# Performance work log

Hardware: AMD Instinct MI355X
Metric: run time of the kernel (lower is better)

The kernel has to match this reference:

```python
import jax, jax.numpy as jnp
import numpy as np

B, C, Hh, Ww = 1, 64, 64, 64
NH, DK = 8, 64
D = NH * DK  # 512


def _gelu(x):
    return jax.nn.gelu(x, approximate=False)


def _dwconv3x3(x, w):
    # x: [b, ch, h, w]; w: [ch, 1, 3, 3] (torch depthwise layout, groups=ch)
    return jax.lax.conv_general_dilated(
        x, w, window_strides=(1, 1), padding='SAME',
        feature_group_count=x.shape[1],
        dimension_numbers=('NCHW', 'OIHW', 'NCHW'))


def _bn(x, g, b, m, v):
    # eval-mode BatchNorm2d, eps=1e-5
    s = (g / jnp.sqrt(v + 1e-5))[None, :, None, None]
    return (x - m[None, :, None, None]) * s + b[None, :, None, None]


def setup_inputs() -> dict:
    key = jax.random.key(0)
    ks = jax.random.split(key, 16)
    r = lambda k, sh, sc=0.02: (jax.random.normal(k, sh, dtype=jnp.float32) * sc)
    return {
        'x_in': jax.random.normal(ks[0], (B, C, Hh, Ww), dtype=jnp.float32),
        'Wq': r(ks[1], (D, C)), 'Wk': r(ks[2], (D, C)), 'Wv': r(ks[3], (D, C)),
        'scale': jnp.ones((NH, 1, 1), dtype=jnp.float32),
        'Wout': r(ks[4], (C, D)), 'bout': jnp.zeros((C,), jnp.float32),
        'dw_w': r(ks[5], (D, 1, 3, 3), 0.1), 'dw_b': jnp.zeros((D,), jnp.float32),
        'dw_g': jnp.ones((D,), jnp.float32), 'dw_bt': jnp.zeros((D,), jnp.float32),
        'dw_m': jnp.zeros((D,), jnp.float32), 'dw_v': jnp.ones((D,), jnp.float32),
        'ci_w1': r(ks[6], (D // 4, D)), 'ci_b1': jnp.zeros((D // 4,), jnp.float32),
        'ci_w2': r(ks[7], (D, D // 4)), 'ci_b2': jnp.zeros((D,), jnp.float32),
        'si_w1': r(ks[8], (D // 16, D)), 'si_b1': jnp.zeros((D // 16,), jnp.float32),
        'si_g': jnp.ones((D // 16,), jnp.float32), 'si_bt': jnp.zeros((D // 16,), jnp.float32),
        'si_m': jnp.zeros((D // 16,), jnp.float32), 'si_v': jnp.ones((D // 16,), jnp.float32),
        'si_w2': r(ks[9], (1, D // 16)), 'si_b2': jnp.zeros((1,), jnp.float32),
        'pe_w1': r(ks[10], (C, 1, 3, 3), 0.1), 'pe_w2': r(ks[11], (C, 1, 3, 3), 0.1),
    }


def reference(x_in, Wq, Wk, Wv, scale, Wout, bout,
              dw_w, dw_b, dw_g, dw_bt, dw_m, dw_v,
              ci_w1, ci_b1, ci_w2, ci_b2,
              si_w1, si_b1, si_g, si_bt, si_m, si_v, si_w2, si_b2,
              pe_w1, pe_w2):
    b, c, h, w = x_in.shape
    n = h * w
    nh, dk = NH, DK
    dh = nh * dk

    x = x_in.reshape(b, c, n).transpose(0, 2, 1)  # [b, n, c]

    q = (x @ Wq.T).reshape(b, n, nh, dk).transpose(0, 2, 1, 3)  # [b,nh,n,dk]
    k = (x @ Wk.T).reshape(b, n, nh, dk).transpose(0, 2, 1, 3)
    v_flat = x @ Wv.T                                            # [b,n,D]
    v = v_flat.reshape(b, n, nh, dk).transpose(0, 2, 1, 3)
    v_img = v_flat.transpose(0, 2, 1).reshape(b, dh, h, w)       # [b,D,h,w]

    # cosine normalization (F.normalize, eps=1e-12)
    q = q / jnp.clip(jnp.linalg.norm(q, axis=-1, keepdims=True), 1e-12)
    k = k / jnp.clip(jnp.linalg.norm(k, axis=-1, keepdims=True), 1e-12)

    dist = jnp.einsum('bhid,bhjd->bhij', q, k) * scale  # scale: [nh,1,1] broadcast
    dist = jax.nn.softmax(dist, axis=-1)
    att = jnp.einsum('bhij,bhjd->bhid', dist, v)          # [b,nh,n,dk]
    att = att.transpose(0, 2, 1, 3).reshape(b, n, dh)     # [b,n,D]

    # depthwise conv branch on v
    conv_x = _gelu(_bn(_dwconv3x3(v_img, dw_w) + dw_b[None, :, None, None],
                       dw_g, dw_bt, dw_m, dw_v))          # [b,D,h,w]

    # channel interaction: global-avg-pool of attention, two 1x1 convs
    pooled = att.mean(axis=1)                             # [b,D] (avg over n == avg over h,w)
    cm = _gelu(pooled @ ci_w1.T + ci_b1) @ ci_w2.T + ci_b2  # [b,D]

    # spatial interaction: 1x1 -> BN -> GELU -> 1x1 on conv branch
    s1 = jnp.einsum('bdhw,ed->behw', conv_x, si_w1) + si_b1[None, :, None, None]
    s1 = _gelu(_bn(s1, si_g, si_bt, si_m, si_v))
    sm = jnp.einsum('behw,oe->bohw', s1, si_w2) + si_b2[None, :, None, None]  # [b,1,h,w]
    sm = sm.transpose(0, 2, 3, 1).reshape(b, n, 1)

    attened = att * jax.nn.sigmoid(sm)
    conv_g = conv_x * jax.nn.sigmoid(cm)[:, :, None, None]
    conv_g = conv_g.transpose(0, 2, 3, 1).reshape(b, n, dh)

    y = (attened + conv_g) @ Wout.T + bout               # [b,n,c]
    out = y.reshape(b, c, h, w)  # faithful to original (no transpose before reshape)

    embed = _dwconv3x3(_gelu(_dwconv3x3(x_in, pe_w1)), pe_w2)
    return out + embed
```

## Files before the change

kernel.cpp:

```cpp
#include <hip/hip_runtime.h>


#define LOG2E 1.442695040888963f

typedef __attribute__((ext_vector_type(8))) short bf16x8;
typedef __attribute__((ext_vector_type(4))) float f32x4;
typedef __attribute__((ext_vector_type(4))) int i32x4;
typedef __attribute__((ext_vector_type(2))) int i32x2;
typedef __attribute__((ext_vector_type(4))) ushort u16x4;

__device__ __forceinline__ ushort f2bf(float x){
  uint u = __float_as_uint(x);
  u += 0x7fffu + ((u >> 16) & 1u);
  return (ushort)(u >> 16);
}
__device__ __forceinline__ float bf2f(ushort h){
  return __uint_as_float(((uint)h) << 16);
}
__device__ __forceinline__ float gelu_(float x){
  return 0.5f * x * (1.0f + erff(x * 0.70710678118654752f));
}
__device__ __forceinline__ float sigmoid_(float x){
  return 1.0f / (1.0f + __expf(-x));
}
__device__ __forceinline__ float exp2_(float x){
  float r; asm("v_exp_f32 %0, %1" : "=v"(r) : "v"(x)); return r;
}
__device__ __forceinline__ int cvtpk(float lo, float hi){
  int r; asm("v_cvt_pk_bf16_f32 %0, %1, %2" : "=v"(r) : "v"(lo), "v"(hi)); return r;
}
__device__ __forceinline__ bf16x8 packf8(const float* s){
  f32x4 x0 = *(const f32x4*)s;
  f32x4 x1 = *(const f32x4*)(s+4);
  union{ i32x4 i; bf16x8 v; } u;
  u.i[0]=cvtpk(x0[0],x0[1]); u.i[1]=cvtpk(x0[2],x0[3]);
  u.i[2]=cvtpk(x1[0],x1[1]); u.i[3]=cvtpk(x1[2],x1[3]);
  return u.v;
}
__device__ __forceinline__ void gload16(const ushort* g, ushort* l){
  __builtin_amdgcn_global_load_lds(
    (const __attribute__((address_space(1))) uint*)(const void*)g,
    (__attribute__((address_space(3))) uint*)(void*)l, 16, 0, 0);
}

__global__ __launch_bounds__(256) void k_qkv(const float* __restrict__ xin,
    const float* __restrict__ Wq, const float* __restrict__ Wk,
    const float* __restrict__ Wv, const float* __restrict__ scale,
    ushort* __restrict__ q_bf, ushort* __restrict__ k_bf, ushort* __restrict__ vT,
    const float* __restrict__ pe_w1, const float* __restrict__ pe_w2,
    float* __restrict__ embed, const float* __restrict__ Wout,
    const float* __restrict__ si_w1, ushort* __restrict__ Woutb,
    ushort* __restrict__ si_w1b, float* __restrict__ pooled){
  __shared__ float t0[20*64];
  __shared__ float t1[18*64];
  const int z = blockIdx.y;
  const int tid = threadIdx.x;
  if (z == 3){
    if (tid < 192){
      int i = blockIdx.x*192 + tid;
      if (i < 32768) Woutb[i] = f2bf(Wout[i]);
      else           si_w1b[i - 32768] = f2bf(si_w1[i - 32768]);
    }
    if (blockIdx.x == 0){ pooled[tid] = 0.f; pooled[tid+256] = 0.f; }
    const int c = blockIdx.x >> 2;
    const int r0 = (blockIdx.x & 3) * 16;
    const float* src = xin + (size_t)c*4096;
#pragma unroll
    for (int i=0;i<5;i++){
      int idx = tid + 256*i;
      if (idx < 1280){
        int lr = idx >> 6, x = idx & 63;
        int gr = r0 - 2 + lr;
        t0[idx] = (gr >= 0 && gr < 64) ? src[gr*64 + x] : 0.f;
      }
    }
    __syncthreads();
    float w1[9], w2[9];
#pragma unroll
    for (int i=0;i<9;i++){ w1[i] = pe_w1[c*9+i]; w2[i] = pe_w2[c*9+i]; }
#pragma unroll
    for (int i=0;i<5;i++){
      int idx = tid + 256*i;
      if (idx < 1152){
        int lr = idx >> 6, x = idx & 63;
        int gr = r0 - 1 + lr;
        float acc = 0.f;
        if (gr >= 0 && gr < 64){
#pragma unroll
          for (int ky=0;ky<3;ky++){
            int gy = gr + ky - 1;
            if (gy < 0 || gy > 63) continue;
#pragma unroll
            for (int kx=0;kx<3;kx++){
              int xx = x + kx - 1;
              if (xx < 0 || xx > 63) continue;
              acc += w1[ky*3+kx] * t0[(lr + ky)*64 + xx];
            }
          }
          acc = gelu_(acc);
        }
        t1[idx] = acc;
      }
    }
    __syncthreads();
    float* dst = embed + (size_t)c*4096;
#pragma unroll
    for (int i=0;i<4;i++){
      int idx = tid + 256*i;
      int lr = idx >> 6, x = idx & 63;
      int gr = r0 + lr;
      float acc = 0.f;
#pragma unroll
      for (int ky=0;ky<3;ky++){
        int gy = gr + ky - 1;
        if (gy < 0 || gy > 63) continue;
#pragma unroll
        for (int kx=0;kx<3;kx++){
          int xx = x + kx - 1;
          if (xx < 0 || xx > 63) continue;
          acc += w2[ky*3+kx] * t1[(lr + ky)*64 + xx];
        }
      }
      dst[gr*64 + x] = acc;
    }
    return;
  }
  const int n0 = blockIdx.x * 16;
  const int lane = tid & 63, w = tid >> 6;
  const int l15 = lane & 15, g = lane >> 4;
  const int obase = w * 128;
  const float* W = (z==0) ? Wq : (z==1) ? Wk : Wv;
  const int n = n0 + l15;
  float xa[8], xc[8];
#pragma unroll
  for (int j=0;j<8;j++){
    xa[j] = xin[(8*g + j)*4096 + n];
    xc[j] = xin[(32 + 8*g + j)*4096 + n];
  }
  union{ i32x4 i; bf16x8 v; } ua, uc;
  ua.i[0]=cvtpk(xa[0],xa[1]); ua.i[1]=cvtpk(xa[2],xa[3]);
  ua.i[2]=cvtpk(xa[4],xa[5]); ua.i[3]=cvtpk(xa[6],xa[7]);
  uc.i[0]=cvtpk(xc[0],xc[1]); uc.i[1]=cvtpk(xc[2],xc[3]);
  uc.i[2]=cvtpk(xc[4],xc[5]); uc.i[3]=cvtpk(xc[6],xc[7]);
  bf16x8 a0 = ua.v, a1 = uc.v;
  f32x4 acc[8];
#pragma unroll
  for (int t=0;t<8;t++) acc[t] = (f32x4){0.f,0.f,0.f,0.f};
#pragma unroll
  for (int t=0;t<8;t++){
    const float* brow = W + (size_t)(obase + 16*t + l15)*64;
    bf16x8 b0 = packf8(brow + 8*g);
    bf16x8 b1 = packf8(brow + 32 + 8*g);
    acc[t] = __builtin_amdgcn_mfma_f32_16x16x32_bf16(a0, b0, acc[t], 0,0,0);
    acc[t] = __builtin_amdgcn_mfma_f32_16x16x32_bf16(a1, b1, acc[t], 0,0,0);
  }
  if (z < 2){
#pragma unroll
    for (int hh=0; hh<2; hh++){
      float sfac = (z==0) ? (scale[2*w+hh] * LOG2E) : 1.0f;
#pragma unroll
      for (int r=0;r<4;r++){
        float ss = 0.f;
#pragma unroll
        for (int tt=0;tt<4;tt++){ float v = acc[hh*4+tt][r]; ss += v*v; }
        ss += __shfl_xor(ss, 1); ss += __shfl_xor(ss, 2);
        ss += __shfl_xor(ss, 4); ss += __shfl_xor(ss, 8);
        float inv = sfac / fmaxf(sqrtf(ss), 1e-12f);
#pragma unroll
        for (int tt=0;tt<4;tt++) acc[hh*4+tt][r] *= inv;
      }
    }
    ushort* dst = (z==0) ? q_bf : k_bf;
#pragma unroll
    for (int t=0;t<8;t++){
      int col = obase + 16*t + l15;
#pragma unroll
      for (int r=0;r<4;r++)
        dst[(size_t)(n0 + 4*g + r)*512 + col] = f2bf(acc[t][r]);
    }
  } else {
#pragma unroll
    for (int t=0;t<8;t++){
      int col = obase + 16*t + l15;
      u16x4 vs;
#pragma unroll
      for (int r=0;r<4;r++) vs[r] = f2bf(acc[t][r]);
      *(u16x4*)(vT + (size_t)col*4096 + n0 + 4*g) = vs;
    }
  }
}

__global__ __launch_bounds__(512) void k_attn_conv(const ushort* __restrict__ q_bf,
    const ushort* __restrict__ k_bf, const ushort* __restrict__ vT,
    ushort* __restrict__ O_part, float* __restrict__ lsum_part, int log2S,
    const float* __restrict__ dw_w, const float* __restrict__ dw_b,
    const float* __restrict__ dw_g, const float* __restrict__ dw_bt,
    const float* __restrict__ dw_m, const float* __restrict__ dw_v,
    ushort* __restrict__ conv_x){
  __shared__ ushort Kt[2][4096];
  __shared__ ushort Vt[2][4096];
  const int S = 1 << log2S;
  const int NA = 128 << log2S;
  const int bid = blockIdx.x;
  const int tid = threadIdx.x;

  if (bid >= NA){
    float* tile = (float*)&Kt[0][0];
    const int d = bid - NA;
    const ushort* src = vT + (size_t)d*4096;
#pragma unroll
    for (int j=0;j<2;j++){
      u16x4 va = *(const u16x4*)(src + tid*4 + 2048*j);
      f32x4 vf;
#pragma unroll
      for (int i=0;i<4;i++) vf[i] = bf2f(va[i]);
      *(f32x4*)&tile[tid*4 + 2048*j] = vf;
    }
    __syncthreads();
    float wv[9];
#pragma unroll
    for (int i=0;i<9;i++) wv[i] = dw_w[d*9+i];
    const float bias = dw_b[d];
    const float bnsc = dw_g[d] * rsqrtf(dw_v[d] + 1e-5f);
    const float bnb  = dw_bt[d] - dw_m[d]*bnsc;
    ushort* dst = conv_x + (size_t)d*4096;
#pragma unroll 4
    for (int i=0;i<8;i++){
      int p = tid + 512*i;
      int y = p >> 6, x = p & 63;
      float acc = 0.f;
#pragma unroll
      for (int ky=0;ky<3;ky++){
        int yy = y + ky - 1;
        if (yy < 0 || yy > 63) continue;
#pragma unroll
        for (int kx=0;kx<3;kx++){
          int xx = x + kx - 1;
          if (xx < 0 || xx > 63) continue;
          acc += wv[ky*3+kx] * tile[yy*64 + xx];
        }
      }
      float cc = (acc + bias)*bnsc + bnb;
      dst[p] = f2bf(gelu_(cc));
    }
    return;
  }
  const int combo = bid & (8*S - 1);
  const int qb = bid >> (3 + log2S);
  const int h = combo >> log2S;
  const int seg = combo & (S - 1);
  const int kv0 = seg * (4096 >> log2S);
  const int iters = (4096 >> log2S) >> 6;
  const int lane = tid & 63, w = tid >> 6;
  const int l15 = lane & 15, g = lane >> 4;

  const int lr8 = lane >> 3;
  const int swzc = ((lane & 7) ^ lr8) << 3;
  const ushort* kSrc = k_bf + (size_t)(kv0 + w*8 + lr8)*512 + h*64 + swzc;
  const ushort* vSrc = vT + (size_t)(h*64 + w*8 + lr8)*4096 + kv0 + swzc;
  ushort* klds[2] = { &Kt[0][w*512], &Kt[1][w*512] };
  ushort* vlds[2] = { &Vt[0][w*512], &Vt[1][w*512] };

  const int qrow0 = qb*256 + w*32;
  bf16x8 qa[2][2];
#pragma unroll
  for (int tq=0;tq<2;tq++){
    const ushort* qrow = q_bf + (size_t)(qrow0 + tq*16 + l15)*512 + h*64;
    qa[tq][0] = *(const bf16x8*)(qrow + 8*g);
    qa[tq][1] = *(const bf16x8*)(qrow + 32 + 8*g);
  }
  f32x4 O[2][4];
#pragma unroll
  for (int tq=0;tq<2;tq++)
#pragma unroll
    for (int t=0;t<4;t++) O[tq][t] = (f32x4){0.f,0.f,0.f,0.f};
  float lsum[2] = {0.f,0.f};

  gload16(kSrc, klds[0]);
  gload16(vSrc, vlds[0]);
  asm volatile("s_waitcnt vmcnt(0)" ::: "memory");
  __builtin_amdgcn_s_barrier();

  const int x7 = l15 & 7;
  const int g2 = g >> 1, gh = (g & 1) << 2;

  for (int it = 0; it < iters; ++it){
    const int buf = it & 1;
    if (it + 1 < iters){
      kSrc += 64*512; vSrc += 64;
      gload16(kSrc, klds[buf^1]);
      gload16(vSrc, vlds[buf^1]);
    }
    const ushort* Kb = Kt[buf];
    const ushort* Vb = Vt[buf];
    i32x4 PA[2][2];
#pragma unroll
    for (int s=0;s<4;s++){
      const int rr = 16*s + l15;
      bf16x8 kf0 = *(const bf16x8*)&Kb[rr*64 + ((g     ^ x7) << 3)];
      bf16x8 kf1 = *(const bf16x8*)&Kb[rr*64 + (((4+g) ^ x7) << 3)];
      const int sp = s >> 1, hi = (s & 1) << 1;
#pragma unroll
      for (int tq=0;tq<2;tq++){
        f32x4 st = (f32x4){0.f,0.f,0.f,0.f};
        st = __builtin_amdgcn_mfma_f32_16x16x32_bf16(kf0, qa[tq][0], st, 0,0,0);
        st = __builtin_amdgcn_mfma_f32_16x16x32_bf16(kf1, qa[tq][1], st, 0,0,0);
        float p0 = exp2_(st[0]), p1 = exp2_(st[1]);
        float p2 = exp2_(st[2]), p3 = exp2_(st[3]);
        lsum[tq] += (p0 + p1) + (p2 + p3);
        PA[tq][sp][hi]   = cvtpk(p0, p1);
        PA[tq][sp][hi+1] = cvtpk(p2, p3);
      }
    }
    __builtin_amdgcn_s_setprio(1);
#pragma unroll
    for (int t=0;t<4;t++){
      const int rr = 16*t + l15;
      union { bf16x8 v; i32x2 h2[2]; } u0, u1;
      u0.h2[0] = *(const i32x2*)&Vb[rr*64 + ((g2       ^ x7) << 3) + gh];
      u0.h2[1] = *(const i32x2*)&Vb[rr*64 + (((2 + g2) ^ x7) << 3) + gh];
      u1.h2[0] = *(const i32x2*)&Vb[rr*64 + (((4 + g2) ^ x7) << 3) + gh];
      u1.h2[1] = *(const i32x2*)&Vb[rr*64 + (((6 + g2) ^ x7) << 3) + gh];
#pragma unroll
      for (int tq=0;tq<2;tq++){
        union { i32x4 i; bf16x8 v; } a0, a1;
        a0.i = PA[tq][0]; a1.i = PA[tq][1];
        O[tq][t] = __builtin_amdgcn_mfma_f32_16x16x32_bf16(a0.v, u0.v, O[tq][t], 0,0,0);
        O[tq][t] = __builtin_amdgcn_mfma_f32_16x16x32_bf16(a1.v, u1.v, O[tq][t], 0,0,0);
      }
    }
    __builtin_amdgcn_s_setprio(0);
    asm volatile("s_waitcnt vmcnt(0)" ::: "memory");
    __builtin_amdgcn_s_barrier();
  }
#pragma unroll
  for (int tq=0;tq<2;tq++){
    float ls = lsum[tq];
    ls += __shfl_xor(ls, 16); ls += __shfl_xor(ls, 32);
    if (g == 0)
      lsum_part[((size_t)seg*8 + h)*4096 + qrow0 + tq*16 + l15] = ls;
  }
  ushort* Op = O_part + (size_t)seg*4096*512;
#pragma unroll
  for (int tq=0;tq<2;tq++)
#pragma unroll
    for (int t=0;t<4;t++)
#pragma unroll
      for (int r=0;r<4;r++)
        Op[(size_t)(qrow0 + tq*16 + 4*g + r)*512 + h*64 + 16*t + l15] = f2bf(O[tq][t][r]);
}

template<int S>
__global__ __launch_bounds__(256) void k_comb_t(const ushort* __restrict__ O_part,
    const float* __restrict__ lsum_part, ushort* __restrict__ att_bf,
    float* __restrict__ pooled){
  __shared__ float Linv[16][8];
  __shared__ float red[4][512];
  const int qbase = blockIdx.x * 16;
  const int tid = threadIdx.x;
  if (tid < 128){
    int q = tid >> 3, h = tid & 7;
    float L = 0.f;
#pragma unroll
    for (int s=0;s<S;s++) L += lsum_part[((size_t)s*8 + h)*4096 + qbase + q];
    Linv[q][h] = 1.0f / L;
  }
  __syncthreads();
  const int ch = tid & 63;
  const int qg = tid >> 6;
  const int d0 = ch * 8;
  const int hh = ch >> 3;
  float pool[8] = {0.f,0.f,0.f,0.f,0.f,0.f,0.f,0.f};
#pragma unroll
  for (int qq=0; qq<4; qq++){
    const int q = qg*4 + qq;
    const size_t idx = (size_t)(qbase + q)*512 + d0;
    i32x4 seg[S];
#pragma unroll
    for (int s=0;s<S;s++)
      seg[s] = *(const i32x4*)(O_part + (size_t)s*4096*512 + idx);
    float o[8];
#pragma unroll
    for (int j=0;j<8;j++){
      uint pk = ((const uint*)&seg[0])[j>>1];
      o[j] = bf2f((ushort)(pk >> ((j&1)*16)));
    }
#pragma unroll
    for (int s=1;s<S;s++)
#pragma unroll
      for (int j=0;j<8;j++){
        uint pk = ((const uint*)&seg[s])[j>>1];
        o[j] += bf2f((ushort)(pk >> ((j&1)*16)));
      }
    const float li = Linv[q][hh];
    union{ i32x4 i; } w;
#pragma unroll
    for (int j=0;j<8;j++){ o[j] *= li; pool[j] += o[j]; }
    w.i[0]=cvtpk(o[0],o[1]); w.i[1]=cvtpk(o[2],o[3]);
    w.i[2]=cvtpk(o[4],o[5]); w.i[3]=cvtpk(o[6],o[7]);
    *(i32x4*)(att_bf + idx) = w.i;
  }
  *(f32x4*)&red[qg][d0]     = *(f32x4*)&pool[0];
  *(f32x4*)&red[qg][d0 + 4] = *(f32x4*)&pool[4];
  __syncthreads();
  {
    int d = tid;
    float s0 = red[0][d] + red[1][d] + red[2][d] + red[3][d];
    int d2 = tid + 256;
    float s1 = red[0][d2] + red[1][d2] + red[2][d2] + red[3][d2];
    atomicAdd(&pooled[d], s0);
    atomicAdd(&pooled[d2], s1);
  }
}

__global__ __launch_bounds__(512) void k_final(const ushort* __restrict__ att_bf,
    const ushort* __restrict__ conv_x, const ushort* __restrict__ si_w1b,
    const float* __restrict__ si_b1, const float* __restrict__ si_g,
    const float* __restrict__ si_bt, const float* __restrict__ si_m,
    const float* __restrict__ si_v, const float* __restrict__ si_w2,
    const float* __restrict__ si_b2,
    const float* __restrict__ pooled, const float* __restrict__ ci_w1,
    const float* __restrict__ ci_b1, const float* __restrict__ ci_w2,
    const float* __restrict__ ci_b2,
    const ushort* __restrict__ Woutb, const float* __restrict__ bout,
    const float* __restrict__ embed, float* __restrict__ out){
  __shared__ ushort ct[16*520];
  __shared__ float pl[512];
  __shared__ float h1[128];
  __shared__ float scm[512];
  __shared__ f32x4 part2[8][2][64];
  __shared__ float smv[16];
  __shared__ f32x4 part[8][4][64];
  const int tid = threadIdx.x;
  const int lane = tid & 63, w = tid >> 6;
  const int l15 = lane & 15, g = lane >> 4;
  const int n0 = blockIdx.x * 16;
  const int rowA = n0 + l15;
  pl[tid] = pooled[tid] * (1.0f/4096.0f);
  {
    const ushort* s = conv_x + (size_t)tid*4096 + n0;
    union{ i32x4 q[2]; ushort e[16]; } u;
    u.q[0] = *(const i32x4*)s;
    u.q[1] = *(const i32x4*)(s + 8);
#pragma unroll
    for (int j=0;j<16;j++) ct[j*520 + tid] = u.e[j];
  }
  bf16x8 at8[2];
#pragma unroll
  for (int kk=0;kk<2;kk++){
    int k0 = w*64 + kk*32 + 8*g;
    at8[kk] = *(const bf16x8*)(att_bf + (size_t)rowA*512 + k0);
  }
  __syncthreads();
  if (tid < 256){
    int e = tid >> 1;
    int base = (tid & 1) * 256;
    float acc = 0.f;
    const float* wr = ci_w1 + (size_t)e*512 + base;
#pragma unroll 8
    for (int c=0;c<256;c++) acc += wr[c]*pl[base + c];
    acc += __shfl_xor(acc, 1);
    if (!(tid & 1)) h1[e] = gelu_(acc + ci_b1[e]);
  }
  bf16x8 cn8[2];
#pragma unroll
  for (int kk=0;kk<2;kk++){
    int k0 = w*64 + kk*32 + 8*g;
    cn8[kk] = *(const bf16x8*)&ct[l15*520 + k0];
  }
  __syncthreads();
  {
    float acc = ci_b2[tid];
    const float* wr = ci_w2 + (size_t)tid*128;
#pragma unroll 8
    for (int e=0;e<128;e++) acc += wr[e]*h1[e];
    scm[tid] = sigmoid_(acc);
  }
  f32x4 a2[2];
  a2[0] = (f32x4){0.f,0.f,0.f,0.f};
  a2[1] = (f32x4){0.f,0.f,0.f,0.f};
#pragma unroll
  for (int kk=0;kk<2;kk++){
    int k0 = w*64 + kk*32 + 8*g;
#pragma unroll
    for (int t=0;t<2;t++){
      bf16x8 b = *(const bf16x8*)(si_w1b + (size_t)(16*t + l15)*512 + k0);
      a2[t] = __builtin_amdgcn_mfma_f32_16x16x32_bf16(cn8[kk], b, a2[t], 0,0,0);
    }
  }
  part2[w][0][lane] = a2[0];
  part2[w][1][lane] = a2[1];
  __syncthreads();
  if (w == 0){
    float rowv[4] = {0.f,0.f,0.f,0.f};
#pragma unroll
    for (int t=0;t<2;t++){
      f32x4 s4 = part2[0][t][lane];
#pragma unroll
      for (int ww=1;ww<8;ww++) s4 = s4 + part2[ww][t][lane];
      int e = 16*t + l15;
      float s = si_g[e] * rsqrtf(si_v[e] + 1e-5f);
      float b1 = si_b1[e] - si_m[e];
      float bt = si_bt[e];
      float w2e = si_w2[e];
#pragma unroll
      for (int r=0;r<4;r++){
        float v = (s4[r] + b1)*s + bt;
        rowv[r] += w2e * gelu_(v);
      }
    }
    float sb2 = si_b2[0];
#pragma unroll
    for (int r=0;r<4;r++){
      float v = rowv[r];
      v += __shfl_xor(v,1); v += __shfl_xor(v,2);
      v += __shfl_xor(v,4); v += __shfl_xor(v,8);
      if (l15 == 0) smv[4*g + r] = sigmoid_(v + sb2);
    }
  }
  __syncthreads();
  const float srow = smv[l15];
  f32x4 acc[4];
#pragma unroll
  for (int t=0;t<4;t++) acc[t] = (f32x4){0.f,0.f,0.f,0.f};
#pragma unroll
  for (int kk=0;kk<2;kk++){
    int k0 = w*64 + kk*32 + 8*g;
    bf16x8 af;
#pragma unroll
    for (int i=0;i<8;i++){
      int d = k0 + i;
      float zv = bf2f((ushort)at8[kk][i]) * srow + bf2f((ushort)cn8[kk][i]) * scm[d];
      af[i] = (short)f2bf(zv);
    }
#pragma unroll
    for (int t=0;t<4;t++){
      bf16x8 bf8 = *(const bf16x8*)(Woutb + (size_t)(16*t+l15)*512 + k0);
      acc[t] = __builtin_amdgcn_mfma_f32_16x16x32_bf16(af, bf8, acc[t], 0,0,0);
    }
  }
#pragma unroll
  for (int t=0;t<4;t++) part[w][t][lane] = acc[t];
  __syncthreads();
  if (w < 4){
    f32x4 s4 = part[0][w][lane];
#pragma unroll
    for (int ww=1;ww<8;ww++) s4 = s4 + part[ww][w][lane];
    int o = 16*w + l15;
    float bo = bout[o];
#pragma unroll
    for (int r=0;r<4;r++){
      int row = n0 + 4*g + r;
      size_t idx = (size_t)row*64 + o;
      out[idx] = s4[r] + bo + embed[idx];
    }
  }
}

extern "C" void kernel_launch(void* const* d_in, const int* in_sizes, int n_in,
                              void* d_out, int out_size, void* d_ws, size_t ws_size,
                              hipStream_t stream){
  (void)in_sizes; (void)n_in; (void)out_size;
  const float* x_in  = (const float*)d_in[0];
  const float* Wq    = (const float*)d_in[1];
  const float* Wk    = (const float*)d_in[2];
  const float* Wv    = (const float*)d_in[3];
  const float* scale = (const float*)d_in[4];
  const float* Wout  = (const float*)d_in[5];
  const float* bout  = (const float*)d_in[6];
  const float* dw_w  = (const float*)d_in[7];
  const float* dw_b  = (const float*)d_in[8];
  const float* dw_g  = (const float*)d_in[9];
  const float* dw_bt = (const float*)d_in[10];
  const float* dw_m  = (const float*)d_in[11];
  const float* dw_v  = (const float*)d_in[12];
  const float* ci_w1 = (const float*)d_in[13];
  const float* ci_b1 = (const float*)d_in[14];
  const float* ci_w2 = (const float*)d_in[15];
  const float* ci_b2 = (const float*)d_in[16];
  const float* si_w1 = (const float*)d_in[17];
  const float* si_b1 = (const float*)d_in[18];
  const float* si_g  = (const float*)d_in[19];
  const float* si_bt = (const float*)d_in[20];
  const float* si_m  = (const float*)d_in[21];
  const float* si_v  = (const float*)d_in[22];
  const float* si_w2 = (const float*)d_in[23];
  const float* si_b2 = (const float*)d_in[24];
  const float* pe_w1 = (const float*)d_in[25];
  const float* pe_w2 = (const float*)d_in[26];
  float* out = (float*)d_out;

  char* p = (char*)d_ws;
  auto alloc = [&](size_t bytes)->char*{
    char* r = p; p += (bytes + 255) & ~(size_t)255; return r;
  };
  ushort* q_bf    = (ushort*)alloc((size_t)4096*512*2);
  ushort* k_bf    = (ushort*)alloc((size_t)4096*512*2);
  ushort* vTb     = (ushort*)alloc((size_t)512*4096*2);
  ushort* att_bf  = (ushort*)alloc((size_t)4096*512*2);
  ushort* conv_x  = (ushort*)alloc((size_t)512*4096*2);
  ushort* Woutb   = (ushort*)alloc((size_t)32768*2);
  ushort* si_w1b  = (ushort*)alloc((size_t)16384*2);
  float*  embed   = (float*) alloc((size_t)64*4096*4);
  float*  lsum_p  = (float*) alloc((size_t)8*8*4096*4);
  float*  pooled  = (float*) alloc(512*4);
  size_t used = (size_t)(p - (char*)d_ws);
  size_t segBytes = (size_t)4096*512*2 + 256;
  size_t avail = (ws_size > used) ? (ws_size - used) : 0;
  int log2S = 2;
  if (avail < 4*segBytes) log2S = 1;
  if (avail < 2*segBytes) log2S = 0;
  int S = 1 << log2S;
  ushort* O_part = (ushort*)alloc((size_t)S*segBytes);
  int NA = 128 << log2S;

  k_qkv<<<dim3(256,4), 256, 0, stream>>>(x_in, Wq, Wk, Wv, scale, q_bf, k_bf, vTb,
                                         pe_w1, pe_w2, embed, Wout, si_w1,
                                         Woutb, si_w1b, pooled);
  k_attn_conv<<<NA + 512, 512, 0, stream>>>(q_bf, k_bf, vTb, O_part, lsum_p, log2S,
                                            dw_w, dw_b, dw_g, dw_bt, dw_m, dw_v,
                                            conv_x);
  if (log2S == 2)
    k_comb_t<4><<<256, 256, 0, stream>>>(O_part, lsum_p, att_bf, pooled);
  else if (log2S == 1)
    k_comb_t<2><<<256, 256, 0, stream>>>(O_part, lsum_p, att_bf, pooled);
  else
    k_comb_t<1><<<256, 256, 0, stream>>>(O_part, lsum_p, att_bf, pooled);
  k_final<<<256, 512, 0, stream>>>(att_bf, conv_x, si_w1b, si_b1, si_g, si_bt,
                                   si_m, si_v, si_w2, si_b2,
                                   pooled, ci_w1, ci_b1, ci_w2, ci_b2,
                                   Woutb, bout, embed, out);
}
```

Measured before the change: 102.6 us.

## Compute channel-interaction MLP once in last combine block instead of per final block

The channel-interaction MLP (pooled -> ci_w1 -> GELU -> ci_w2 -> sigmoid) moves out of k_final, where each of the 256 blocks recomputed it redundantly. It now runs once in the last-arriving k_comb block, found with an atomic counter and a threadfence, and the result is written to a global scm buffer. k_comb also switches to 512 blocks of 8 rows each to spread the work across more blocks. The cost is a serialized tail in one block plus more pooled atomics, in exchange for a shorter k_final prologue.

```diff
diff --git a/kernel.cpp b/kernel.cpp
--- a/kernel.cpp
+++ b/kernel.cpp
@@ -50,7 +50,8 @@
     const float* __restrict__ pe_w1, const float* __restrict__ pe_w2,
     float* __restrict__ embed, const float* __restrict__ Wout,
     const float* __restrict__ si_w1, ushort* __restrict__ Woutb,
-    ushort* __restrict__ si_w1b, float* __restrict__ pooled){
+    ushort* __restrict__ si_w1b, float* __restrict__ pooled,
+    uint* __restrict__ cnt){
   __shared__ float t0[20*64];
   __shared__ float t1[18*64];
   const int z = blockIdx.y;
@@ -61,7 +62,10 @@
       if (i < 32768) Woutb[i] = f2bf(Wout[i]);
       else           si_w1b[i - 32768] = f2bf(si_w1[i - 32768]);
     }
-    if (blockIdx.x == 0){ pooled[tid] = 0.f; pooled[tid+256] = 0.f; }
+    if (blockIdx.x == 0){
+      pooled[tid] = 0.f; pooled[tid+256] = 0.f;
+      if (tid == 0) cnt[0] = 0u;
+    }
     const int c = blockIdx.x >> 2;
     const int r0 = (blockIdx.x & 3) * 16;
     const float* src = xin + (size_t)c*4096;
@@ -353,12 +357,17 @@
 template<int S>
 __global__ __launch_bounds__(256) void k_comb_t(const ushort* __restrict__ O_part,
     const float* __restrict__ lsum_part, ushort* __restrict__ att_bf,
-    float* __restrict__ pooled){
-  __shared__ float Linv[16][8];
+    float* __restrict__ pooled, uint* __restrict__ cnt,
+    const float* __restrict__ ci_w1, const float* __restrict__ ci_b1,
+    const float* __restrict__ ci_w2, const float* __restrict__ ci_b2,
+    float* __restrict__ scm){
+  __shared__ float Linv[8][8];
   __shared__ float red[4][512];
-  const int qbase = blockIdx.x * 16;
+  __shared__ float h1[128];
+  __shared__ uint lastflag;
+  const int qbase = blockIdx.x * 8;
   const int tid = threadIdx.x;
-  if (tid < 128){
+  if (tid < 64){
     int q = tid >> 3, h = tid & 7;
     float L = 0.f;
 #pragma unroll
@@ -372,8 +381,8 @@
   const int hh = ch >> 3;
   float pool[8] = {0.f,0.f,0.f,0.f,0.f,0.f,0.f,0.f};
 #pragma unroll
-  for (int qq=0; qq<4; qq++){
-    const int q = qg*4 + qq;
+  for (int qq=0; qq<2; qq++){
+    const int q = qg*2 + qq;
     const size_t idx = (size_t)(qbase + q)*512 + d0;
     i32x4 seg[S];
 #pragma unroll
@@ -393,12 +402,12 @@
         o[j] += bf2f((ushort)(pk >> ((j&1)*16)));
       }
     const float li = Linv[q][hh];
-    union{ i32x4 i; } w;
+    union{ i32x4 i; } wpk;
 #pragma unroll
     for (int j=0;j<8;j++){ o[j] *= li; pool[j] += o[j]; }
-    w.i[0]=cvtpk(o[0],o[1]); w.i[1]=cvtpk(o[2],o[3]);
-    w.i[2]=cvtpk(o[4],o[5]); w.i[3]=cvtpk(o[6],o[7]);
-    *(i32x4*)(att_bf + idx) = w.i;
+    wpk.i[0]=cvtpk(o[0],o[1]); wpk.i[1]=cvtpk(o[2],o[3]);
+    wpk.i[2]=cvtpk(o[4],o[5]); wpk.i[3]=cvtpk(o[6],o[7]);
+    *(i32x4*)(att_bf + idx) = wpk.i;
   }
   *(f32x4*)&red[qg][d0]     = *(f32x4*)&pool[0];
   *(f32x4*)&red[qg][d0 + 4] = *(f32x4*)&pool[4];
@@ -411,6 +420,34 @@
     atomicAdd(&pooled[d], s0);
     atomicAdd(&pooled[d2], s1);
   }
+  __threadfence();
+  if (tid == 0) lastflag = atomicAdd(cnt, 1u);
+  __syncthreads();
+  if (lastflag != 511u) return;
+  float* pl = red[0];
+  pl[tid]       = atomicAdd(&pooled[tid], 0.f)       * (1.0f/4096.0f);
+  pl[tid + 256] = atomicAdd(&pooled[tid + 256], 0.f) * (1.0f/4096.0f);
+  __syncthreads();
+  {
+    int e = tid >> 1;
+    int base = (tid & 1) * 256;
+    float acc = 0.f;
+    const float* wr = ci_w1 + (size_t)e*512 + base;
+#pragma unroll 8
+    for (int c=0;c<256;c++) acc += wr[c]*pl[base + c];
+    acc += __shfl_xor(acc, 1);
+    if (!(tid & 1)) h1[e] = gelu_(acc + ci_b1[e]);
+  }
+  __syncthreads();
+#pragma unroll
+  for (int dd=0; dd<2; dd++){
+    int d = tid + 256*dd;
+    float acc = ci_b2[d];
+    const float* wr = ci_w2 + (size_t)d*128;
+#pragma unroll 8
+    for (int e=0;e<128;e++) acc += wr[e]*h1[e];
+    scm[d] = sigmoid_(acc);
+  }
 }
 
 __global__ __launch_bounds__(512) void k_final(const ushort* __restrict__ att_bf,
@@ -418,16 +455,11 @@
     const float* __restrict__ si_b1, const float* __restrict__ si_g,
     const float* __restrict__ si_bt, const float* __restrict__ si_m,
     const float* __restrict__ si_v, const float* __restrict__ si_w2,
-    const float* __restrict__ si_b2,
-    const float* __restrict__ pooled, const float* __restrict__ ci_w1,
-    const float* __restrict__ ci_b1, const float* __restrict__ ci_w2,
-    const float* __restrict__ ci_b2,
+    const float* __restrict__ si_b2, const float* __restrict__ scm,
     const ushort* __restrict__ Woutb, const float* __restrict__ bout,
     const float* __restrict__ embed, float* __restrict__ out){
   __shared__ ushort ct[16*520];
-  __shared__ float pl[512];
-  __shared__ float h1[128];
-  __shared__ float scm[512];
+  __shared__ float scml[512];
   __shared__ f32x4 part2[8][2][64];
   __shared__ float smv[16];
   __shared__ f32x4 part[8][4][64];
@@ -436,7 +468,7 @@
   const int l15 = lane & 15, g = lane >> 4;
   const int n0 = blockIdx.x * 16;
   const int rowA = n0 + l15;
-  pl[tid] = pooled[tid] * (1.0f/4096.0f);
+  scml[tid] = scm[tid];
   {
     const ushort* s = conv_x + (size_t)tid*4096 + n0;
     union{ i32x4 q[2]; ushort e[16]; } u;
@@ -452,29 +484,11 @@
     at8[kk] = *(const bf16x8*)(att_bf + (size_t)rowA*512 + k0);
   }
   __syncthreads();
-  if (tid < 256){
-    int e = tid >> 1;
-    int base = (tid & 1) * 256;
-    float acc = 0.f;
-    const float* wr = ci_w1 + (size_t)e*512 + base;
-#pragma unroll 8
-    for (int c=0;c<256;c++) acc += wr[c]*pl[base + c];
-    acc += __shfl_xor(acc, 1);
-    if (!(tid & 1)) h1[e] = gelu_(acc + ci_b1[e]);
-  }
   bf16x8 cn8[2];
 #pragma unroll
   for (int kk=0;kk<2;kk++){
     int k0 = w*64 + kk*32 + 8*g;
     cn8[kk] = *(const bf16x8*)&ct[l15*520 + k0];
-  }
-  __syncthreads();
-  {
-    float acc = ci_b2[tid];
-    const float* wr = ci_w2 + (size_t)tid*128;
-#pragma unroll 8
-    for (int e=0;e<128;e++) acc += wr[e]*h1[e];
-    scm[tid] = sigmoid_(acc);
   }
   f32x4 a2[2];
   a2[0] = (f32x4){0.f,0.f,0.f,0.f};
@@ -530,7 +544,7 @@
 #pragma unroll
     for (int i=0;i<8;i++){
       int d = k0 + i;
-      float zv = bf2f((ushort)at8[kk][i]) * srow + bf2f((ushort)cn8[kk][i]) * scm[d];
+      float zv = bf2f((ushort)at8[kk][i]) * srow + bf2f((ushort)cn8[kk][i]) * scml[d];
       af[i] = (short)f2bf(zv);
     }
 #pragma unroll
@@ -604,6 +618,8 @@
   float*  embed   = (float*) alloc((size_t)64*4096*4);
   float*  lsum_p  = (float*) alloc((size_t)8*8*4096*4);
   float*  pooled  = (float*) alloc(512*4);
+  float*  scm     = (float*) alloc(512*4);
+  uint*   cnt     = (uint*)  alloc(256);
   size_t used = (size_t)(p - (char*)d_ws);
   size_t segBytes = (size_t)4096*512*2 + 256;
   size_t avail = (ws_size > used) ? (ws_size - used) : 0;
@@ -616,18 +632,20 @@
 
   k_qkv<<<dim3(256,4), 256, 0, stream>>>(x_in, Wq, Wk, Wv, scale, q_bf, k_bf, vTb,
                                          pe_w1, pe_w2, embed, Wout, si_w1,
-                                         Woutb, si_w1b, pooled);
+                                         Woutb, si_w1b, pooled, cnt);
   k_attn_conv<<<NA + 512, 512, 0, stream>>>(q_bf, k_bf, vTb, O_part, lsum_p, log2S,
                                             dw_w, dw_b, dw_g, dw_bt, dw_m, dw_v,
                                             conv_x);
   if (log2S == 2)
-    k_comb_t<4><<<256, 256, 0, stream>>>(O_part, lsum_p, att_bf, pooled);
+    k_comb_t<4><<<512, 256, 0, stream>>>(O_part, lsum_p, att_bf, pooled, cnt,
+                                         ci_w1, ci_b1, ci_w2, ci_b2, scm);
   else if (log2S == 1)
-    k_comb_t<2><<<256, 256, 0, stream>>>(O_part, lsum_p, att_bf, pooled);
+    k_comb_t<2><<<512, 256, 0, stream>>>(O_part, lsum_p, att_bf, pooled, cnt,
+                                         ci_w1, ci_b1, ci_w2, ci_b2, scm);
   else
-    k_comb_t<1><<<256, 256, 0, stream>>>(O_part, lsum_p, att_bf, pooled);
+    k_comb_t<1><<<512, 256, 0, stream>>>(O_part, lsum_p, att_bf, pooled, cnt,
+                                         ci_w1, ci_b1, ci_w2, ci_b2, scm);
   k_final<<<256, 512, 0, stream>>>(att_bf, conv_x, si_w1b, si_b1, si_g, si_bt,
-                                   si_m, si_v, si_w2, si_b2,
-                                   pooled, ci_w1, ci_b1, ci_w2, ci_b2,
+                                   si_m, si_v, si_w2, si_b2, scm,
                                    Woutb, bout, embed, out);
 }
```

Result: slower. 145.5 us (+41.8%).
